# Kernel optimization log

Hardware: AMD Instinct MI355X
Metric: run time of the kernel (lower is better)

## Reference

```python
import jax, jax.numpy as jnp
import numpy as np
import math

N_H = 16

def _rope(x):
    # x: [b, h, n, d_k]; standard RoPE with half-split rotation
    n, d_k = x.shape[2], x.shape[3]
    inv_freq = 1.0 / (10000.0 ** (jnp.arange(0, d_k, 2, dtype=jnp.float32) / d_k))  # [d_k/2]
    freqs = jnp.arange(n, dtype=jnp.float32)[:, None] * inv_freq[None, :]            # [n, d_k/2]
    cos = jnp.concatenate([jnp.cos(freqs), jnp.cos(freqs)], axis=-1)[None, None]     # [1,1,n,d_k]
    sin = jnp.concatenate([jnp.sin(freqs), jnp.sin(freqs)], axis=-1)[None, None]
    x1, x2 = jnp.split(x, 2, axis=-1)
    rot = jnp.concatenate([-x2, x1], axis=-1)
    return x * cos + rot * sin


def setup_inputs() -> dict:
    key = jax.random.key(0)
    k1, k2, k3, k4 = jax.random.split(key, 4)
    b, n, d_m = 2, 1024, 2048
    x = jax.random.normal(k1, (b, n, d_m), dtype=jnp.float32)
    # causal mask (1 = keep, 0 = masked)
    m = jnp.tril(jnp.ones((n, n), dtype=jnp.int32))[None, None]  # [1,1,n,n]
    s = 1.0 / math.sqrt(d_m)
    Wqkv = jax.random.normal(k2, (d_m, 3 * d_m), dtype=jnp.float32) * s
    Wout = jax.random.normal(k3, (d_m, d_m), dtype=jnp.float32) * s
    bout = jax.random.normal(k4, (d_m,), dtype=jnp.float32) * 0.01
    return {"x": x, "m": m, "Wqkv": Wqkv, "Wout": Wout, "bout": bout}


def reference(x, m, Wqkv, Wout, bout):
    b, n, d = x.shape
    d_k = d // N_H
    qkv = (x @ Wqkv).reshape(b, n, 3, N_H, d_k)
    qkv = jnp.transpose(qkv, (2, 0, 3, 1, 4))  # [3, b, h, n, d_k]
    q, k, v = qkv[0], qkv[1], qkv[2]
    q, k = _rope(q), _rope(k)
    s = jnp.einsum('bhqd,bhkd->bhqk', q, k) / math.sqrt(d_k)
    s = jnp.where(m == 0, -jnp.inf, s)
    a = jax.nn.softmax(s, axis=-1)  # dropout is identity in eval / drop=0
    r = jnp.einsum('bhqk,bhkd->bhqd', a, v)
    r = jnp.transpose(r, (0, 2, 1, 3)).reshape(b, n, d)
    return r @ Wout + bout
```

## Files before the change

### kernel.cpp

```cpp
#include <hip/hip_runtime.h>
#include <math.h>

typedef unsigned short u16;
typedef unsigned int u32;
typedef __attribute__((ext_vector_type(8))) short short8;
typedef __attribute__((ext_vector_type(4))) float f32x4;

#define DEVI __device__ __forceinline__

DEVI u16 f2bf(float x) {
    union { float f; u32 u; } un; un.f = x;
    u32 u = un.u;
    return (u16)((u + 0x7fffu + ((u >> 16) & 1u)) >> 16);
}
DEVI float bf2f(u16 v) {
    union { u32 u; float f; } un; un.u = ((u32)v) << 16;
    return un.f;
}
DEVI f32x4 mfma_bf16(short8 a, short8 b, f32x4 c) {
    return __builtin_amdgcn_mfma_f32_16x16x32_bf16(a, b, c, 0, 0, 0);
}
DEVI void gload_lds16(const void* g, void* l) {
    __builtin_amdgcn_global_load_lds((const __attribute__((address_space(1))) u32*)g,
                                     (__attribute__((address_space(3))) u32*)l,
                                     16, 0, 0);
}

__global__ void k_prep(const float* __restrict__ x, const float* __restrict__ Wqkv,
                       const float* __restrict__ Wout, u16* __restrict__ x_bf,
                       u16* __restrict__ WqkvT, u16* __restrict__ WoutT) {
    __shared__ u16 tile[64][68];
    const int bid = blockIdx.x;
    if (bid < 4096) {
        long idx = ((long)bid * 256 + threadIdx.x) * 4;
        float4 v = *(const float4*)(x + idx);
        ushort4 o;
        o.x = f2bf(v.x); o.y = f2bf(v.y); o.z = f2bf(v.z); o.w = f2bf(v.w);
        *(ushort4*)(x_bf + idx) = o;
        return;
    }
    const float* in;
    u16* out;
    int R, C, bx, by;
    if (bid < 7168) {
        int lb = bid - 4096;
        in = Wqkv; out = WqkvT; R = 2048; C = 6144;
        bx = lb % 96; by = lb / 96;
    } else {
        int lb = bid - 7168;
        in = Wout; out = WoutT; R = 2048; C = 2048;
        bx = lb & 31; by = lb >> 5;
    }
    const int tx = threadIdx.x & 15, ty = threadIdx.x >> 4;
    const long r0 = (long)by * 64, c0 = (long)bx * 64;
#pragma unroll
    for (int p = 0; p < 4; ++p) {
        int r = ty + p * 16;
        float4 v = *(const float4*)(in + (r0 + r) * C + c0 + tx * 4);
        ushort4 o;
        o.x = f2bf(v.x); o.y = f2bf(v.y); o.z = f2bf(v.z); o.w = f2bf(v.w);
        *(ushort4*)&tile[r][tx * 4] = o;
    }
    __syncthreads();
#pragma unroll
    for (int p = 0; p < 4; ++p) {
        int rr = ty + p * 16;
        ushort4 o;
        o.x = tile[tx * 4 + 0][rr];
        o.y = tile[tx * 4 + 1][rr];
        o.z = tile[tx * 4 + 2][rr];
        o.w = tile[tx * 4 + 3][rr];
        *(ushort4*)(out + (c0 + rr) * R + r0 + tx * 4) = o;
    }
}

template <int EPI, int TM>
__global__ __launch_bounds__(256, 3) void k_gemm(const u16* __restrict__ A,
                                                 const u16* __restrict__ BT, int K,
                                                 u16* __restrict__ qb, u16* __restrict__ kb,
                                                 u16* __restrict__ vtb, float* __restrict__ out,
                                                 const float* __restrict__ bias) {
    constexpr int MI = TM / 32;
    constexpr int CA = TM / 32;
    __shared__ __align__(16) union SM {
        struct { u16 As[TM * 64]; u16 Bs[128 * 64]; } s;
        u16 T[EPI == 0 ? 128 * 132 : 8];
    } sm;
    const int tid = threadIdx.x;
    const int lane = tid & 63, wave = tid >> 6;
    const int lm = lane & 15, quad = lane >> 4;
    const int wm = wave >> 1, wn = wave & 1;
    const int bm = blockIdx.x, bn = blockIdx.y;

    f32x4 acc[MI][4] = {};

    const int srow = lane >> 3;
    const int scb = (lane & 7) ^ srow;
    const long arow0 = (long)bm * TM;
    const long brow0 = (long)bn * 128;

    for (int k0 = 0; k0 < K; k0 += 64) {
        __syncthreads();
#pragma unroll
        for (int it = 0; it < CA; ++it) {
            int ch = wave * CA + it;
            long r = ch * 8 + srow;
            gload_lds16(A + (arow0 + r) * K + k0 + scb * 8, (char*)sm.s.As + ch * 1024);
        }
#pragma unroll
        for (int it = 0; it < 4; ++it) {
            int ch = wave * 4 + it;
            long r = ch * 8 + srow;
            gload_lds16(BT + (brow0 + r) * K + k0 + scb * 8, (char*)sm.s.Bs + ch * 1024);
        }
        __syncthreads();
#pragma unroll
        for (int ko = 0; ko < 2; ++ko) {
            short8 af[MI], bf[4];
#pragma unroll
            for (int i = 0; i < MI; ++i) {
                int row = wm * (TM / 2) + i * 16 + lm;
                int pc = (ko * 4 + quad) ^ (lm & 7);
                af[i] = *(const short8*)&sm.s.As[row * 64 + pc * 8];
            }
#pragma unroll
            for (int j = 0; j < 4; ++j) {
                int row = wn * 64 + j * 16 + lm;
                int pc = (ko * 4 + quad) ^ (lm & 7);
                bf[j] = *(const short8*)&sm.s.Bs[row * 64 + pc * 8];
            }
#pragma unroll
            for (int i = 0; i < MI; ++i)
#pragma unroll
                for (int j = 0; j < 4; ++j)
                    acc[i][j] = mfma_bf16(af[i], bf[j], acc[i][j]);
        }
    }

    if constexpr (EPI == 0) {
        __syncthreads();
#pragma unroll
        for (int i = 0; i < MI; ++i)
#pragma unroll
            for (int j = 0; j < 4; ++j) {
                const int col = wn * 64 + j * 16 + lm;
#pragma unroll
                for (int r = 0; r < 4; ++r) {
                    const int row = wm * 64 + i * 16 + quad * 4 + r;
                    sm.T[row * 132 + col] = f2bf(acc[i][j][r]);
                }
            }
        __syncthreads();
        const int which = bn >> 4, h = bn & 15, b = bm >> 3;
        const int p0 = (bm & 7) * 128;
        if (which < 2) {
            u16* dst = which ? kb : qb;
            const long hb = ((long)(b * 16 + h)) * 1024;
            const int i0 = (tid * 4) & 63;
            const int pb = tid >> 4;
            float inv[4];
#pragma unroll
            for (int e = 0; e < 4; ++e)
                inv[e] = exp2f(-(float)(i0 + e) * 0.20762050593045952f);
#pragma unroll
            for (int c = 0; c < 8; ++c) {
                const int pos_l = c * 16 + pb;
                ushort4 cur = *(const ushort4*)&sm.T[pos_l * 132 + i0];
                ushort4 par = *(const ushort4*)&sm.T[pos_l * 132 + i0 + 64];
                const float pg = (float)(p0 + pos_l);
                ushort4 o1, o2;
                const u16* cp = (const u16*)&cur;
                const u16* pp = (const u16*)&par;
                u16* o1p = (u16*)&o1;
                u16* o2p = (u16*)&o2;
#pragma unroll
                for (int e = 0; e < 4; ++e) {
                    float th = pg * inv[e];
                    float sv = __sinf(th), cv = __cosf(th);
                    float x1 = bf2f(cp[e]), x2 = bf2f(pp[e]);
                    o1p[e] = f2bf(x1 * cv - x2 * sv);
                    o2p[e] = f2bf(x2 * cv + x1 * sv);
                }
                const long rowb = (hb + p0 + pos_l) * 128;
                *(ushort4*)(dst + rowb + i0) = o1;
                *(ushort4*)(dst + rowb + i0 + 64) = o2;
            }
        } else {
            const long vrow = ((long)(b * 16 + h)) * 128;
#pragma unroll
            for (int c = 0; c < 8; ++c) {
                const int lin = c * 2048 + tid * 8;
                const int dk = lin >> 7;
                const int ps = lin & 127;
                ushort4 o1, o2;
                u16* o1p = (u16*)&o1;
                u16* o2p = (u16*)&o2;
#pragma unroll
                for (int e = 0; e < 4; ++e) {
                    o1p[e] = sm.T[(ps + e) * 132 + dk];
                    o2p[e] = sm.T[(ps + 4 + e) * 132 + dk];
                }
                u16* dst = vtb + (vrow + dk) * 1024 + p0 + ps;
                *(ushort4*)dst = o1;
                *(ushort4*)(dst + 4) = o2;
            }
        }
    } else {
        float bv[4];
#pragma unroll
        for (int j = 0; j < 4; ++j) bv[j] = bias[bn * 128 + wn * 64 + j * 16 + lm];
#pragma unroll
        for (int i = 0; i < MI; ++i) {
#pragma unroll
            for (int r = 0; r < 4; ++r) {
                const int row = bm * TM + wm * (TM / 2) + i * 16 + quad * 4 + r;
#pragma unroll
                for (int j = 0; j < 4; ++j) {
                    const int col = bn * 128 + wn * 64 + j * 16 + lm;
                    out[(long)row * 2048 + col] = acc[i][j][r] + bv[j];
                }
            }
        }
    }
}

__global__ __launch_bounds__(256, 3) void k_flash(const u16* __restrict__ Q,
                                                  const u16* __restrict__ Kb,
                                                  const u16* __restrict__ VT,
                                                  u16* __restrict__ R) {
    __shared__ u16 Ks[64 * 128];
    __shared__ u16 Vs[128 * 64];
    __shared__ u16 Ps[64 * 72];
    const int tid = threadIdx.x;
    const int lane = tid & 63, wave = tid >> 6;
    const int lm = lane & 15, quad = lane >> 4;
    const int id = blockIdx.x;
    const int g = id >> 8, rem = id & 255;
    const int bh = rem >> 3, s = rem & 7;
    const int qt = g ? (15 - s) : s;
    const long qkbase = (long)bh * 1024 * 128;
    const long vtbase = (long)bh * 128 * 1024;
    const int q0 = qt * 64;

    short8 qf[4];
    {
        const u16* qrow = Q + qkbase + (long)(q0 + wave * 16 + lm) * 128 + quad * 8;
#pragma unroll
        for (int kc = 0; kc < 4; ++kc) qf[kc] = *(const short8*)(qrow + kc * 32);
    }

    f32x4 o_acc[8] = {};
    float m_i = -INFINITY, l_i = 0.f;
    const float cl2e = 0.08838834764831845f * 1.4426950408889634f;

    const int kr = lane >> 4;
    const int vr = lane >> 3;
    const int vcb = (lane & 7) ^ vr;

    for (int kt = 0; kt <= qt; ++kt) {
        __syncthreads();
        {
#pragma unroll
            for (int it = 0; it < 4; ++it) {
                int ch = wave * 4 + it;
                int krow = ch * 4 + kr;
                int kchunk = (lane & 15) ^ (krow & 15);
                gload_lds16(Kb + qkbase + (long)(kt * 64 + krow) * 128 + kchunk * 8,
                            (char*)Ks + ch * 1024);
                int vrow = ch * 8 + vr;
                gload_lds16(VT + vtbase + (long)vrow * 1024 + kt * 64 + vcb * 8,
                            (char*)Vs + ch * 1024);
            }
        }
        __syncthreads();

        f32x4 s_acc[4] = {};
#pragma unroll
        for (int kc = 0; kc < 4; ++kc) {
#pragma unroll
            for (int mi = 0; mi < 4; ++mi) {
                int row = mi * 16 + lm;
                int pc = (kc * 4 + quad) ^ lm;
                short8 ak = *(const short8*)&Ks[row * 128 + pc * 8];
                s_acc[mi] = mfma_bf16(ak, qf[kc], s_acc[mi]);
            }
        }
        const int qg = q0 + wave * 16 + lm;
        float t[4][4];
        float cmax = -INFINITY;
#pragma unroll
        for (int mi = 0; mi < 4; ++mi)
#pragma unroll
            for (int r = 0; r < 4; ++r) {
                int kg = kt * 64 + mi * 16 + quad * 4 + r;
                float val = (kg <= qg) ? s_acc[mi][r] * cl2e : -INFINITY;
                t[mi][r] = val;
                cmax = fmaxf(cmax, val);
            }
        cmax = fmaxf(cmax, __shfl_xor(cmax, 16));
        cmax = fmaxf(cmax, __shfl_xor(cmax, 32));
        float m_new = fmaxf(m_i, cmax);
        float alpha = exp2f(m_i - m_new);
        float csum = 0.f;
#pragma unroll
        for (int mi = 0; mi < 4; ++mi)
#pragma unroll
            for (int r = 0; r < 4; ++r) {
                float p = exp2f(t[mi][r] - m_new);
                t[mi][r] = p;
                csum += p;
            }
        csum += __shfl_xor(csum, 16);
        csum += __shfl_xor(csum, 32);
        l_i = l_i * alpha + csum;
        m_i = m_new;
#pragma unroll
        for (int mi = 0; mi < 4; ++mi) {
            ushort4 pk;
            pk.x = f2bf(t[mi][0]); pk.y = f2bf(t[mi][1]);
            pk.z = f2bf(t[mi][2]); pk.w = f2bf(t[mi][3]);
            *(ushort4*)&Ps[(wave * 16 + lm) * 72 + mi * 16 + quad * 4] = pk;
        }
        float aq[4];
#pragma unroll
        for (int r = 0; r < 4; ++r) aq[r] = __shfl(alpha, quad * 4 + r, 64);
#pragma unroll
        for (int nt = 0; nt < 8; ++nt)
#pragma unroll
            for (int r = 0; r < 4; ++r) o_acc[nt][r] *= aq[r];
#pragma unroll
        for (int kc = 0; kc < 2; ++kc) {
            short8 ap = *(const short8*)&Ps[(wave * 16 + lm) * 72 + kc * 32 + quad * 8];
#pragma unroll
            for (int nt = 0; nt < 8; ++nt) {
                int row = nt * 16 + lm;
                int pc = (kc * 4 + quad) ^ (lm & 7);
                short8 bv = *(const short8*)&Vs[row * 64 + pc * 8];
                o_acc[nt] = mfma_bf16(ap, bv, o_acc[nt]);
            }
        }
    }
    float lq[4];
#pragma unroll
    for (int r = 0; r < 4; ++r) lq[r] = __shfl(l_i, quad * 4 + r, 64);
    const int b = bh >> 4, h = bh & 15;
#pragma unroll
    for (int nt = 0; nt < 8; ++nt)
#pragma unroll
        for (int r = 0; r < 4; ++r) {
            const int pos = q0 + wave * 16 + quad * 4 + r;
            const int col = h * 128 + nt * 16 + lm;
            R[((long)b * 1024 + pos) * 2048 + col] = f2bf(o_acc[nt][r] / lq[r]);
        }
}

extern "C" void kernel_launch(void* const* d_in, const int* in_sizes, int n_in,
                              void* d_out, int out_size, void* d_ws, size_t ws_size,
                              hipStream_t stream) {
    const float* x    = (const float*)d_in[0];
    const float* Wqkv = (const float*)d_in[2];
    const float* Wout = (const float*)d_in[3];
    const float* bout = (const float*)d_in[4];
    float* out = (float*)d_out;

    char* ws = (char*)d_ws;
    u16* x_bf  = (u16*)(ws);
    u16* rbuf  = x_bf;
    u16* WqkvT = (u16*)(ws + (8L << 20));
    u16* WoutT = (u16*)(ws + (32L << 20));
    u16* qbuf  = (u16*)(ws + (40L << 20));
    u16* kbuf  = (u16*)(ws + (48L << 20));
    u16* vtbuf = (u16*)(ws + (56L << 20));

    k_prep<<<8192, 256, 0, stream>>>(x, Wqkv, Wout, x_bf, WqkvT, WoutT);
    k_gemm<0, 128><<<dim3(16, 48), 256, 0, stream>>>(x_bf, WqkvT, 2048, qbuf, kbuf, vtbuf,
                                                     nullptr, nullptr);
    k_flash<<<512, 256, 0, stream>>>(qbuf, kbuf, vtbuf, rbuf);
    k_gemm<1, 64><<<dim3(32, 16), 256, 0, stream>>>(rbuf, WoutT, 2048, nullptr, nullptr,
                                                    nullptr, out, bout);
}
```

Before: 237.5 us.

## Replace QKV GEMM with 256x256-tile, 8-wave double-buffered pipelined kernel

Adds a dedicated QKV projection kernel that uses 256x256 output tiles with 512 threads. It double-buffers A/B tiles in LDS via direct global-to-LDS loads, interleaving quarter-tile loads with MFMA quadrants and raising wave priority around the MFMAs. The RoPE/V-transpose epilogue is adapted to process two heads per block in two halves. The aim is more operand reuse per LDS byte and overlap of memory with compute, at the cost of 192 blocks (fewer than the CU count) and higher register/LDS pressure.

```diff
diff --git a/kernel.cpp b/kernel.cpp
--- a/kernel.cpp
+++ b/kernel.cpp
@@ -72,6 +72,196 @@
         o.w = tile[tx * 4 + 3][rr];
         *(ushort4*)(out + (c0 + rr) * R + r0 + tx * 4) = o;
     }
+}
+
+__global__ __launch_bounds__(512, 2) void k_qkv256(const u16* __restrict__ A,
+                                                   const u16* __restrict__ BT,
+                                                   u16* __restrict__ qb, u16* __restrict__ kb,
+                                                   u16* __restrict__ vtb) {
+    constexpr int K = 2048, NT = K / 64;
+    __shared__ __align__(16) union SM {
+        struct { u16 As[2][256 * 64]; u16 Bs[2][256 * 64]; } s;
+        u16 T[128 * 264];
+    } sm;
+    const int tid = threadIdx.x;
+    const int lane = tid & 63, wave = tid >> 6;
+    const int lm = lane & 15, quad = lane >> 4;
+    const int wm = wave >> 2, wn = wave & 3;
+    const int bm = blockIdx.x, bn = blockIdx.y;
+    const int srow = lane >> 3;
+    const int scb = (lane & 7) ^ srow;
+    const long arow0 = (long)bm * 256;
+    const long brow0 = (long)bn * 256;
+
+    f32x4 acc[8][4] = {};
+    short8 a[8], b[4];
+
+    auto stage = [&](const u16* __restrict__ src, long row0, u16* lds, int h, int kt) {
+#pragma unroll
+        for (int it = 0; it < 2; ++it) {
+            int ch = wave * 2 + it;
+            long r = h * 128 + ch * 8 + srow;
+            gload_lds16(src + (row0 + r) * K + (long)kt * 64 + scb * 8,
+                        (char*)lds + h * 16384 + ch * 1024);
+        }
+    };
+    auto ldA = [&](int buf, int h) {
+#pragma unroll
+        for (int ii = 0; ii < 4; ++ii) {
+            int row = h * 128 + wm * 64 + ii * 16 + lm;
+#pragma unroll
+            for (int ks = 0; ks < 2; ++ks) {
+                int pc = (ks * 4 + quad) ^ (lm & 7);
+                a[ii * 2 + ks] = *(const short8*)&sm.s.As[buf][row * 64 + pc * 8];
+            }
+        }
+    };
+    auto ldB = [&](int buf, int h) {
+#pragma unroll
+        for (int jj = 0; jj < 2; ++jj) {
+            int row = h * 128 + wn * 32 + jj * 16 + lm;
+#pragma unroll
+            for (int ks = 0; ks < 2; ++ks) {
+                int pc = (ks * 4 + quad) ^ (lm & 7);
+                b[jj * 2 + ks] = *(const short8*)&sm.s.Bs[buf][row * 64 + pc * 8];
+            }
+        }
+    };
+    auto mmaq = [&](int ih, int jh) {
+        __builtin_amdgcn_s_setprio(1);
+#pragma unroll
+        for (int ks = 0; ks < 2; ++ks)
+#pragma unroll
+            for (int ii = 0; ii < 4; ++ii)
+#pragma unroll
+                for (int jj = 0; jj < 2; ++jj)
+                    acc[ih * 4 + ii][jh * 2 + jj] = mfma_bf16(
+                        a[ii * 2 + ks], b[jj * 2 + ks], acc[ih * 4 + ii][jh * 2 + jj]);
+        __builtin_amdgcn_s_setprio(0);
+    };
+
+#define VMW(n) asm volatile("s_waitcnt vmcnt(" #n ")" ::: "memory")
+#define LGK0 asm volatile("s_waitcnt lgkmcnt(0)" ::: "memory")
+#define BAR                            \
+    do {                               \
+        __builtin_amdgcn_s_barrier();  \
+        asm volatile("" ::: "memory"); \
+    } while (0)
+
+    stage(A, arow0, sm.s.As[0], 0, 0);
+    stage(BT, brow0, sm.s.Bs[0], 0, 0);
+    stage(A, arow0, sm.s.As[0], 1, 0);
+    stage(BT, brow0, sm.s.Bs[0], 1, 0);
+    VMW(4);
+    BAR;
+
+    for (int t = 0; t < NT; ++t) {
+        const int cur = t & 1, nxt = cur ^ 1;
+        const int tn = (t + 1 < NT) ? t + 1 : t;
+        ldA(cur, 0); ldB(cur, 0);
+        stage(A, arow0, sm.s.As[nxt], 0, tn);
+        BAR; LGK0;
+        mmaq(0, 0);
+        VMW(4);
+        BAR;
+        ldA(cur, 1);
+        stage(BT, brow0, sm.s.Bs[nxt], 0, tn);
+        BAR; LGK0;
+        mmaq(1, 0);
+        VMW(4);
+        BAR;
+        ldB(cur, 1);
+        stage(A, arow0, sm.s.As[nxt], 1, tn);
+        BAR; LGK0;
+        mmaq(1, 1);
+        BAR;
+        ldA(cur, 0);
+        stage(BT, brow0, sm.s.Bs[nxt], 1, tn);
+        BAR; LGK0;
+        mmaq(0, 1);
+        VMW(4);
+        BAR;
+    }
+    VMW(0);
+    BAR;
+
+    const int which = bn >> 3;
+    const int hh = tid >> 8, t8 = tid & 255;
+    const int h = (bn & 7) * 2 + hh;
+#pragma unroll
+    for (int rh = 0; rh < 2; ++rh) {
+#pragma unroll
+        for (int ii = 0; ii < 4; ++ii) {
+            const int i = rh * 4 + ii;
+            const int row_l = wm * 64 + ii * 16 + quad * 4;
+#pragma unroll
+            for (int j = 0; j < 4; ++j) {
+                const int col_l = (j < 2 ? wn * 32 + j * 16 : 128 + wn * 32 + (j - 2) * 16) + lm;
+#pragma unroll
+                for (int r = 0; r < 4; ++r)
+                    sm.T[(row_l + r) * 264 + col_l] = f2bf(acc[i][j][r]);
+            }
+        }
+        __syncthreads();
+        const int tb = bm * 256 + rh * 128;
+        const int b_ = tb >> 10, p0 = tb & 1023;
+        if (which < 2) {
+            u16* dst = which ? kb : qb;
+            const long hb = ((long)(b_ * 16 + h)) * 1024;
+            const int i0 = (t8 * 4) & 63;
+            const int pb = t8 >> 4;
+            float inv[4];
+#pragma unroll
+            for (int e = 0; e < 4; ++e)
+                inv[e] = exp2f(-(float)(i0 + e) * 0.20762050593045952f);
+#pragma unroll
+            for (int c = 0; c < 8; ++c) {
+                const int pos_l = c * 16 + pb;
+                ushort4 cu = *(const ushort4*)&sm.T[pos_l * 264 + hh * 128 + i0];
+                ushort4 pa = *(const ushort4*)&sm.T[pos_l * 264 + hh * 128 + i0 + 64];
+                const float pg = (float)(p0 + pos_l);
+                ushort4 o1, o2;
+                const u16* cp = (const u16*)&cu;
+                const u16* pp = (const u16*)&pa;
+                u16* o1p = (u16*)&o1;
+                u16* o2p = (u16*)&o2;
+#pragma unroll
+                for (int e = 0; e < 4; ++e) {
+                    float th = pg * inv[e];
+                    float sv = __sinf(th), cv = __cosf(th);
+                    float x1 = bf2f(cp[e]), x2 = bf2f(pp[e]);
+                    o1p[e] = f2bf(x1 * cv - x2 * sv);
+                    o2p[e] = f2bf(x2 * cv + x1 * sv);
+                }
+                const long rowb = (hb + p0 + pos_l) * 128;
+                *(ushort4*)(dst + rowb + i0) = o1;
+                *(ushort4*)(dst + rowb + i0 + 64) = o2;
+            }
+        } else {
+            const long vrow = ((long)(b_ * 16 + h)) * 128;
+#pragma unroll
+            for (int c = 0; c < 8; ++c) {
+                const int lin = c * 2048 + t8 * 8;
+                const int dk = lin >> 7;
+                const int ps = lin & 127;
+                ushort4 o1, o2;
+                u16* o1p = (u16*)&o1;
+                u16* o2p = (u16*)&o2;
+#pragma unroll
+                for (int e = 0; e < 4; ++e) {
+                    o1p[e] = sm.T[(ps + e) * 264 + hh * 128 + dk];
+                    o2p[e] = sm.T[(ps + 4 + e) * 264 + hh * 128 + dk];
+                }
+                u16* dstv = vtb + (vrow + dk) * 1024 + p0 + ps;
+                *(ushort4*)dstv = o1;
+                *(ushort4*)(dstv + 4) = o2;
+            }
+        }
+        if (rh == 0) __syncthreads();
+    }
+#undef VMW
+#undef LGK0
+#undef BAR
 }
 
 template <int EPI, int TM>
@@ -137,75 +327,7 @@
         }
     }
 
-    if constexpr (EPI == 0) {
-        __syncthreads();
-#pragma unroll
-        for (int i = 0; i < MI; ++i)
-#pragma unroll
-            for (int j = 0; j < 4; ++j) {
-                const int col = wn * 64 + j * 16 + lm;
-#pragma unroll
-                for (int r = 0; r < 4; ++r) {
-                    const int row = wm * 64 + i * 16 + quad * 4 + r;
-                    sm.T[row * 132 + col] = f2bf(acc[i][j][r]);
-                }
-            }
-        __syncthreads();
-        const int which = bn >> 4, h = bn & 15, b = bm >> 3;
-        const int p0 = (bm & 7) * 128;
-        if (which < 2) {
-            u16* dst = which ? kb : qb;
-            const long hb = ((long)(b * 16 + h)) * 1024;
-            const int i0 = (tid * 4) & 63;
-            const int pb = tid >> 4;
-            float inv[4];
-#pragma unroll
-            for (int e = 0; e < 4; ++e)
-                inv[e] = exp2f(-(float)(i0 + e) * 0.20762050593045952f);
-#pragma unroll
-            for (int c = 0; c < 8; ++c) {
-                const int pos_l = c * 16 + pb;
-                ushort4 cur = *(const ushort4*)&sm.T[pos_l * 132 + i0];
-                ushort4 par = *(const ushort4*)&sm.T[pos_l * 132 + i0 + 64];
-                const float pg = (float)(p0 + pos_l);
-                ushort4 o1, o2;
-                const u16* cp = (const u16*)&cur;
-                const u16* pp = (const u16*)&par;
-                u16* o1p = (u16*)&o1;
-                u16* o2p = (u16*)&o2;
-#pragma unroll
-                for (int e = 0; e < 4; ++e) {
-                    float th = pg * inv[e];
-                    float sv = __sinf(th), cv = __cosf(th);
-                    float x1 = bf2f(cp[e]), x2 = bf2f(pp[e]);
-                    o1p[e] = f2bf(x1 * cv - x2 * sv);
-                    o2p[e] = f2bf(x2 * cv + x1 * sv);
-                }
-                const long rowb = (hb + p0 + pos_l) * 128;
-                *(ushort4*)(dst + rowb + i0) = o1;
-                *(ushort4*)(dst + rowb + i0 + 64) = o2;
-            }
-        } else {
-            const long vrow = ((long)(b * 16 + h)) * 128;
-#pragma unroll
-            for (int c = 0; c < 8; ++c) {
-                const int lin = c * 2048 + tid * 8;
-                const int dk = lin >> 7;
-                const int ps = lin & 127;
-                ushort4 o1, o2;
-                u16* o1p = (u16*)&o1;
-                u16* o2p = (u16*)&o2;
-#pragma unroll
-                for (int e = 0; e < 4; ++e) {
-                    o1p[e] = sm.T[(ps + e) * 132 + dk];
-                    o2p[e] = sm.T[(ps + 4 + e) * 132 + dk];
-                }
-                u16* dst = vtb + (vrow + dk) * 1024 + p0 + ps;
-                *(ushort4*)dst = o1;
-                *(ushort4*)(dst + 4) = o2;
-            }
-        }
-    } else {
+    if constexpr (EPI == 1) {
         float bv[4];
 #pragma unroll
         for (int j = 0; j < 4; ++j) bv[j] = bias[bn * 128 + wn * 64 + j * 16 + lm];
@@ -373,8 +495,7 @@
     u16* vtbuf = (u16*)(ws + (56L << 20));
 
     k_prep<<<8192, 256, 0, stream>>>(x, Wqkv, Wout, x_bf, WqkvT, WoutT);
-    k_gemm<0, 128><<<dim3(16, 48), 256, 0, stream>>>(x_bf, WqkvT, 2048, qbuf, kbuf, vtbuf,
-                                                     nullptr, nullptr);
+    k_qkv256<<<dim3(8, 24), 512, 0, stream>>>(x_bf, WqkvT, qbuf, kbuf, vtbuf);
     k_flash<<<512, 256, 0, stream>>>(qbuf, kbuf, vtbuf, rbuf);
     k_gemm<1, 64><<<dim3(32, 16), 256, 0, stream>>>(rbuf, WoutT, 2048, nullptr, nullptr,
                                                     nullptr, out, bout);
```

Result: slower. 255.4 us (+7.5%).
